# Kernel optimization log

Hardware: AMD Instinct MI355X
Metric: run time of the kernel (lower is better)

Reference implementation:

```python
import jax, jax.numpy as jnp
import numpy as np

# ---- config mirroring DetectionPostProcessV1 init + quant params ----
B, H, W, A, C = 8, 128, 128, 8, 8      # batch, feature HxW, anchors/cell, num_classes
STRIDE = 8
IMG_W, IMG_H = 1024, 1024               # image_size
INPUT_SHIFT = 4                          # kInputShift -> in_scale = 1/16
EXP_SHIFT = 4                            # from _gen_exp_table with in_scale 1/16
BOX_THR_INT = 9                          # ceil(0.55 * 2**INPUT_SHIFT)
NMS_THR = 128.0 / 256.0                  # ceil(0.5 * 2**kNmsThresholdShift) / 2**8
NMS_MARGIN = 0.0                         # nms_margin (quantized: ceil(0*16)/16)
PRE_K, POST_K = 1024, 300                # pre-NMS candidates, post_nms_top_k
CLASS_OFFSETS = jnp.zeros((C,), jnp.int32)
CLASS_SEP = 4096.0                       # coordinate offset for class-aware NMS


def setup_inputs() -> dict:
    key = jax.random.key(0)
    k1, _ = jax.random.split(key)
    # int8 repr of quantized head outputs (stored as int32 for jax indexing)
    data = jax.random.randint(k1, (B, A * (4 + C), H, W), -128, 128, dtype=jnp.int32)
    # grid anchors: 8 sizes per cell, stride-8 feature map
    sizes = np.array([16, 24, 32, 48, 64, 96, 128, 192], np.float32)
    ys = (np.arange(H, dtype=np.float32) + 0.5) * STRIDE
    xs = (np.arange(W, dtype=np.float32) + 0.5) * STRIDE
    cy, cx = np.meshgrid(ys, xs, indexing="ij")
    cx, cy = cx[..., None], cy[..., None]              # [H,W,1]
    w = np.broadcast_to(sizes, (H, W, A))
    h = np.broadcast_to(sizes, (H, W, A))
    anchors = np.stack([cx - w / 2, cy - h / 2, cx + w / 2, cy + h / 2], -1)
    anchors = jnp.asarray(anchors.reshape(-1, 4).astype(np.float32))  # [N,4] matches [H,W,A] flatten order
    # integer exp table, exactly as _gen_exp_table
    in_scale = 1.0 / (1 << INPUT_SHIFT)
    idx = np.arange(-128, 128, dtype=np.float32) * in_scale
    ev = np.exp(idx)
    exp_table = jnp.asarray(np.round(ev * (1 << EXP_SHIFT)).astype(np.int32))
    return {"data": data, "anchors": anchors, "exp_table": exp_table}


def _post_process(data, anchors, exp_table):
    N = H * W * A
    # [B, A*(4+C), H, W] -> [B, N, 4+C]
    x = data.reshape(B, A, 4 + C, H, W).transpose(0, 3, 4, 1, 2).reshape(B, N, 4 + C)
    box_d = x[..., :4]
    scores_i = x[..., 4:] + CLASS_OFFSETS                      # int scores with class offsets
    # decode: dx,dy via fixed-point shift; dw,dh via int exp table lookup
    dxy = box_d[..., :2].astype(jnp.float32) / (1 << INPUT_SHIFT)
    expv = exp_table[box_d[..., 2:4] + 128].astype(jnp.float32) / (1 << EXP_SHIFT)
    ctr = (anchors[:, :2] + anchors[:, 2:]) * 0.5              # [N,2]
    wh = anchors[:, 2:] - anchors[:, :2]
    pc = ctr + dxy * wh                                        # [B,N,2]
    pwh = wh * expv
    boxes = jnp.concatenate([pc - pwh * 0.5, pc + pwh * 0.5], -1)
    boxes = jnp.clip(boxes, 0.0, jnp.array([IMG_W, IMG_H, IMG_W, IMG_H], jnp.float32))
    # score filter
    best = scores_i.max(-1)
    label = scores_i.argmax(-1).astype(jnp.int32)
    valid = best >= BOX_THR_INT
    score = best.astype(jnp.float32) / (1 << INPUT_SHIFT)
    sc_masked = jnp.where(valid, score, -1e9)
    topv, topi = jax.lax.top_k(sc_masked, PRE_K)               # [B,PRE_K]
    bk = jnp.take_along_axis(boxes, topi[..., None], 1)        # [B,PRE_K,4]
    lk = jnp.take_along_axis(label, topi, 1)
    vk = topv > -1e8
    # class-aware NMS via coordinate offset trick
    ob = bk + lk[..., None].astype(jnp.float32) * CLASS_SEP
    area = (ob[..., 2] - ob[..., 0]) * (ob[..., 3] - ob[..., 1])
    lt = jnp.maximum(ob[:, :, None, :2], ob[:, None, :, :2])
    rb = jnp.minimum(ob[:, :, None, 2:], ob[:, None, :, 2:])
    whi = jnp.clip(rb - lt, 0.0)
    inter = whi[..., 0] * whi[..., 1]
    iou = inter / (area[:, :, None] + area[:, None, :] - inter + 1e-9)  # [B,PRE_K,PRE_K]
    idxr = jnp.arange(PRE_K)

    def body(i, sup):
        alive_i = ~jnp.take(sup, i, axis=1)                    # [B]
        iou_i = jnp.take(iou, i, axis=1)                       # [B,PRE_K]
        s_i = jnp.take(topv, i, axis=1)[:, None]
        cond = (alive_i[:, None] & (iou_i > NMS_THR)
                & (topv <= s_i - NMS_MARGIN) & (idxr > i)[None, :])
        return sup | cond

    sup = jax.lax.fori_loop(0, PRE_K, body, ~vk)
    keep = vk & ~sup
    fs = jnp.where(keep, topv, -1e9)
    outv, outi = jax.lax.top_k(fs, POST_K)
    boxes_out = jnp.take_along_axis(bk, outi[..., None], 1)
    labels = jnp.take_along_axis(lk, outi, 1)
    ok = outv > -1e8
    boxes_out = jnp.where(ok[..., None], boxes_out, 0.0)       # [B,POST_K,4]
    scores_out = jnp.where(ok, outv, 0.0)                      # [B,POST_K]
    labels_out = jnp.where(ok, labels, -1)                     # [B,POST_K]
    return boxes_out, scores_out, labels_out


def reference(data, anchors, exp_table):
    return _post_process(data, anchors, exp_table)
```

## Files before the change

kernel.cpp:

```cpp
#include <hip/hip_runtime.h>
#include <stdint.h>

#define Bb 8
#define PREK 1024
#define POSTK 300
#define NBIN 120
#define NCHUNK 512

__device__ __forceinline__ float clampb(float v){ return fminf(fmaxf(v, 0.0f), 1024.0f); }

__global__ void __launch_bounds__(256) k1_scores(const int* __restrict__ data,
                                                 unsigned short* __restrict__ sc16,
                                                 int* __restrict__ chist){
    int blk = blockIdx.x;
    int b = blk >> 7, h = blk & 127;
    int tid = threadIdx.x;
    int a = tid >> 5, wg = tid & 31;
    int w = wg << 2;
    const int* p = data + (((size_t)(b*96 + a*12 + 4)) << 14) + (h << 7) + w;
    int4 m = *(const int4*)p;
    int4 lb = make_int4(0,0,0,0);
#pragma unroll
    for (int c = 1; c < 8; ++c){
        int4 v = *(const int4*)(p + ((size_t)c << 14));
        if (v.x > m.x){ m.x = v.x; lb.x = c; }
        if (v.y > m.y){ m.y = v.y; lb.y = c; }
        if (v.z > m.z){ m.z = v.z; lb.z = c; }
        if (v.w > m.w){ m.w = v.w; lb.w = c; }
    }
    ushort4 st;
    st.x = (unsigned short)(((m.x + 128) << 8) | lb.x);
    st.y = (unsigned short)(((m.y + 128) << 8) | lb.y);
    st.z = (unsigned short)(((m.z + 128) << 8) | lb.z);
    st.w = (unsigned short)(((m.w + 128) << 8) | lb.w);
    *(ushort4*)(sc16 + (((size_t)(b*8 + a)) << 14) + (h << 7) + w) = st;

    __shared__ int hist[4][NBIN];
    for (int i = tid; i < 4*NBIN; i += 256) ((int*)hist)[i] = 0;
    __syncthreads();
    int q = wg >> 3;
    if (m.x >= 9) atomicAdd(&hist[q][m.x-9], 1);
    if (m.y >= 9) atomicAdd(&hist[q][m.y-9], 1);
    if (m.z >= 9) atomicAdd(&hist[q][m.z-9], 1);
    if (m.w >= 9) atomicAdd(&hist[q][m.w-9], 1);
    __syncthreads();
    int* cb = chist + ((size_t)(b*NCHUNK + h*4)) * NBIN;
    for (int i = tid; i < 4*NBIN; i += 256) cb[i] = ((int*)hist)[i];
}

__global__ void __launch_bounds__(256) k2_select(int* __restrict__ chist, int* __restrict__ gt,
                                                 int* __restrict__ Tb_, int* __restrict__ dmeta){
    int b = blockIdx.x, tid = threadIdx.x;
    __shared__ int hs2[2][NBIN];
    __shared__ int suf[128];
    __shared__ int Tsh;
    __shared__ int sb[512];
    if (tid == 0) Tsh = -1;
    int half = tid >> 7, bin = tid & 127;
    const int* cb = chist + (size_t)b * NCHUNK * NBIN;
    if (bin < NBIN){
        int s = 0;
        const int* p2 = cb + (size_t)half*256*NBIN + bin;
#pragma unroll 8
        for (int ch = 0; ch < 256; ++ch) s += p2[(size_t)ch * NBIN];
        hs2[half][bin] = s;
    }
    __syncthreads();
    int hbin = 0;
    if (tid < 128){
        hbin = (tid < NBIN) ? hs2[0][tid] + hs2[1][tid] : 0;
        suf[tid] = hbin;
    }
    __syncthreads();
    for (int off = 1; off < 128; off <<= 1){
        int v = 0;
        if (tid < 128 && tid + off < 128) v = suf[tid + off];
        __syncthreads();
        if (tid < 128) suf[tid] += v;
        __syncthreads();
    }
    if (tid < NBIN){
        gt[b*128 + tid] = suf[tid] - hbin;
        if (suf[tid] >= PREK) atomicMax(&Tsh, tid);
    }
    __syncthreads();
    int T = Tsh > 0 ? Tsh : 0;
    if (tid == 0) Tb_[b] = T;
    for (int k = tid; k < PREK; k += 256) dmeta[b*PREK + k] = -1;
    int i0 = tid, i1 = tid + 256;
    for (int abin = T; abin < NBIN; ++abin){
        int* basep = chist + (size_t)(b*NCHUNK) * NBIN + abin;
        int v0 = basep[(size_t)i0 * NBIN], v1 = basep[(size_t)i1 * NBIN];
        sb[i0] = v0; sb[i1] = v1;
        __syncthreads();
        for (int off = 1; off < 512; off <<= 1){
            int a0 = (i0 >= off) ? sb[i0 - off] : 0;
            int a1 = (i1 >= off) ? sb[i1 - off] : 0;
            __syncthreads();
            sb[i0] += a0; sb[i1] += a1;
            __syncthreads();
        }
        basep[(size_t)i0 * NBIN] = sb[i0] - v0;
        basep[(size_t)i1 * NBIN] = sb[i1] - v1;
        __syncthreads();
    }
}

__global__ void __launch_bounds__(256) k3_rank(const unsigned short* __restrict__ sc16,
                                               const int* __restrict__ chist,
                                               const int* __restrict__ gt, const int* __restrict__ Tb_,
                                               const int* __restrict__ data,
                                               const float* __restrict__ anchors,
                                               const int* __restrict__ etab,
                                               float4* __restrict__ dbox, int* __restrict__ dmeta){
    int blk = blockIdx.x;
    int b = blk >> 9, ci = blk & 511;
    int tid = threadIdx.x;
    int h = ci >> 2, w0 = (ci & 3) << 5;
    __shared__ unsigned short sc[256];
    __shared__ int wcnt[4][NBIN];
    if (tid < 64){
        int a = tid & 7, wq = tid >> 3;
        ushort4 v4 = *(const ushort4*)(sc16 + (((size_t)(b*8 + a)) << 14) + (h << 7) + w0 + (wq << 2));
        sc[(wq*4 + 0)*8 + a] = v4.x;
        sc[(wq*4 + 1)*8 + a] = v4.y;
        sc[(wq*4 + 2)*8 + a] = v4.z;
        sc[(wq*4 + 3)*8 + a] = v4.w;
    }
    for (int i = tid; i < 4*NBIN; i += 256) ((int*)wcnt)[i] = 0;
    int T = Tb_[b];
    __syncthreads();
    unsigned short v = sc[tid];
    int s = (int)(v >> 8) - 128;
    int bin = s - 9;
    bool qual = (bin >= T);
    int wv = tid >> 6, lane = tid & 63;
    if (qual) atomicAdd(&wcnt[wv][bin], 1);
    __syncthreads();
    int myeq = 0;
    {
        unsigned long long low = (1ull << lane) - 1ull;
        for (int vb = T; vb < NBIN; ++vb){
            unsigned long long bal = __ballot(qual && bin == vb);
            if (!bal) continue;
            if (qual && bin == vb) myeq = __popcll(bal & low);
        }
    }
    if (!qual) return;
    int cross = 0;
    for (int w2 = 0; w2 < wv; ++w2) cross += wcnt[w2][bin];
    int rank = gt[b*128 + bin] + chist[((size_t)(b*NCHUNK) + ci)*NBIN + bin] + cross + myeq;
    if (rank < PREK){
        int n = ci*256 + tid;
        int a = n & 7, wc = (n >> 3) & 127;
        const int* p = data + (((size_t)(b*96 + a*12)) << 14) + (h << 7) + wc;
        int d0 = p[0], d1 = p[1 << 14], d2 = p[2 << 14], d3 = p[3 << 14];
        float4 an = ((const float4*)anchors)[n];
        float cx = __fmul_rn(__fadd_rn(an.x, an.z), 0.5f);
        float cy = __fmul_rn(__fadd_rn(an.y, an.w), 0.5f);
        float wx = __fsub_rn(an.z, an.x), wy = __fsub_rn(an.w, an.y);
        float dx = __fmul_rn((float)d0, 0.0625f), dy = __fmul_rn((float)d1, 0.0625f);
        float ex = __fmul_rn((float)etab[d2 + 128], 0.0625f);
        float ey = __fmul_rn((float)etab[d3 + 128], 0.0625f);
        float pcx = __fadd_rn(cx, __fmul_rn(dx, wx));
        float pcy = __fadd_rn(cy, __fmul_rn(dy, wy));
        float hx = __fmul_rn(__fmul_rn(wx, ex), 0.5f);
        float hy = __fmul_rn(__fmul_rn(wy, ey), 0.5f);
        float x1 = clampb(__fsub_rn(pcx, hx)), y1 = clampb(__fsub_rn(pcy, hy));
        float x2 = clampb(__fadd_rn(pcx, hx)), y2 = clampb(__fadd_rn(pcy, hy));
        dbox[b*PREK + rank] = make_float4(x1, y1, x2, y2);
        dmeta[b*PREK + rank] = (int)v;
    }
}

__global__ void __launch_bounds__(1024) k45_nms_out(const float4* __restrict__ dbox,
                                                    const int* __restrict__ dmeta,
                                                    float* __restrict__ out){
    int b = blockIdx.x, tid = threadIdx.x, lane = tid & 63, wv = tid >> 6;
    __shared__ float X1[1024], Y1[1024], X2[1024], Y2[1024], AR[1024];
    __shared__ unsigned char KEEP[1024];
    __shared__ int wq[16][8];
    __shared__ int cbs[8], ccn[8];
    __shared__ int wcn[16];
    __shared__ int totS;

    int v = dmeta[b*PREK + tid];
    float4 bb = dbox[b*PREK + tid];
    bool valid = (v >= 0);
    int lc = valid ? (v & 255) : -1;
    float sval = valid ? __fmul_rn((float)((v >> 8) - 128), 0.0625f) : 0.0f;
    KEEP[tid] = 0;
    int win = 0;
#pragma unroll
    for (int c = 0; c < 8; ++c){
        unsigned long long bal = __ballot(lc == c);
        if (lane == 0) wq[wv][c] = __popcll(bal);
        if (lc == c) win = __popcll(bal & ((1ull << lane) - 1ull));
    }
    __syncthreads();
    if (tid < 8){
        int run = 0;
        for (int w2 = 0; w2 < 16; ++w2){ int t = wq[w2][tid]; wq[w2][tid] = run; run += t; }
        ccn[tid] = run;
    }
    __syncthreads();
    if (tid == 0){
        int run = 0;
        for (int c = 0; c < 8; ++c){ cbs[c] = run; run += ccn[c]; }
    }
    __syncthreads();
    int p = 0;
    if (valid){
        p = cbs[lc] + wq[wv][lc] + win;
        float off = (float)(lc << 12);
        float ox1 = __fadd_rn(bb.x, off), oy1 = __fadd_rn(bb.y, off);
        float ox2 = __fadd_rn(bb.z, off), oy2 = __fadd_rn(bb.w, off);
        X1[p] = ox1; Y1[p] = oy1; X2[p] = ox2; Y2[p] = oy2;
        AR[p] = __fmul_rn(__fsub_rn(ox2, ox1), __fsub_rn(oy2, oy1));
    }
    __syncthreads();

    if (wv < 8){
        int M = ccn[wv], base = cbs[wv];
        if (M > 0 && M <= 256){
            float rx1[4], ry1[4], rx2[4], ry2[4], rar[4];
#pragma unroll
            for (int g = 0; g < 4; ++g){
                int r = g*64 + lane;
                int ad = base + ((r < M) ? r : 0);
                rx1[g]=X1[ad]; ry1[g]=Y1[ad]; rx2[g]=X2[ad]; ry2[g]=Y2[ad]; rar[g]=AR[ad];
            }
            unsigned long long mk[4][4];
#pragma unroll
            for (int g = 0; g < 4; ++g)
#pragma unroll
                for (int w2 = 0; w2 < 4; ++w2) mk[g][w2] = 0ull;

#pragma unroll
            for (int jw = 0; jw < 4; ++jw){
                if (jw*64 < M){
                    int lim = M - jw*64; if (lim > 64) lim = 64;
                    for (int jl = 0; jl < lim; ++jl){
                        int j = jw*64 + jl;
                        int aj = base + j;
                        float jx1 = X1[aj], jy1 = Y1[aj], jx2 = X2[aj], jy2 = Y2[aj], jar = AR[aj];
#pragma unroll
                        for (int g = 0; g < 4; ++g){
                            if (g*64 < M){
                                int i = g*64 + lane;
                                float wx = fmaxf(__fsub_rn(fminf(rx2[g], jx2), fmaxf(rx1[g], jx1)), 0.0f);
                                float wy = fmaxf(__fsub_rn(fminf(ry2[g], jy2), fmaxf(ry1[g], jy1)), 0.0f);
                                float inter = __fmul_rn(wx, wy);
                                float den = __fadd_rn(__fsub_rn(__fadd_rn(rar[g], jar), inter), 1e-9f);
                                bool o = (__fdiv_rn(inter, den) > 0.5f) && (j > i);
                                mk[g][jw] |= o ? (1ull << jl) : 0ull;
                            }
                        }
                    }
                }
            }

            unsigned long long r0=0ull, r1=0ull, r2=0ull, r3=0ull;
#pragma unroll
            for (int iw = 0; iw < 4; ++iw){
                if (iw*64 < M){
                    int lim = M - iw*64; if (lim > 64) lim = 64;
                    for (int il = 0; il < lim; ++il){
                        unsigned long long cur = (iw==0)?r0:(iw==1)?r1:(iw==2)?r2:r3;
                        if (!((cur >> il) & 1ull)){
                            unsigned long long w0 = __shfl(mk[iw][0], il);
                            unsigned long long w1 = __shfl(mk[iw][1], il);
                            unsigned long long w2_ = __shfl(mk[iw][2], il);
                            unsigned long long w3_ = __shfl(mk[iw][3], il);
                            r0 |= w0; r1 |= w1; r2 |= w2_; r3 |= w3_;
                        }
                    }
                }
            }
#pragma unroll
            for (int g = 0; g < 4; ++g){
                int r = g*64 + lane;
                unsigned long long rg = (g==0)?r0:(g==1)?r1:(g==2)?r2:r3;
                if (r < M) KEEP[base + r] = (unsigned char)(((rg >> lane) & 1ull) ^ 1ull);
            }
        } else if (M > 256){
            for (int m = lane; m < M; m += 64) KEEP[base+m] = 0;
            for (int i = 0; i < M; ++i){
                if (KEEP[base+i]) continue;
                float xi1 = X1[base+i], yi1 = Y1[base+i];
                float xi2 = X2[base+i], yi2 = Y2[base+i], ai = AR[base+i];
                for (int j = i + 1 + lane; j < M; j += 64){
                    if (KEEP[base+j]) continue;
                    float wx = fmaxf(__fsub_rn(fminf(xi2, X2[base+j]), fmaxf(xi1, X1[base+j])), 0.0f);
                    float wy = fmaxf(__fsub_rn(fminf(yi2, Y2[base+j]), fmaxf(yi1, Y1[base+j])), 0.0f);
                    float inter = __fmul_rn(wx, wy);
                    float den = __fadd_rn(__fsub_rn(__fadd_rn(ai, AR[base+j]), inter), 1e-9f);
                    if (__fdiv_rn(inter, den) > 0.5f) KEEP[base+j] = 1;
                }
            }
            for (int m = lane; m < M; m += 64) KEEP[base+m] ^= 1;
        }
    }
    __syncthreads();

    bool kp = valid && (KEEP[p] != 0);
    unsigned long long bal = __ballot(kp);
    if (lane == 0) wcn[wv] = __popcll(bal);
    __syncthreads();
    if (tid == 0){
        int r = 0;
        for (int w2 = 0; w2 < 16; ++w2){ int t = wcn[w2]; wcn[w2] = r; r += t; }
        totS = r;
    }
    __syncthreads();
    int pos = wcn[wv] + __popcll(bal & ((1ull << lane) - 1ull));
    float* boxes  = out;
    float* scores = out + Bb*POSTK*4;
    float* labs   = out + Bb*POSTK*5;
    if (kp && pos < POSTK){
        int o = (b*POSTK + pos)*4;
        boxes[o+0] = bb.x; boxes[o+1] = bb.y; boxes[o+2] = bb.z; boxes[o+3] = bb.w;
        scores[b*POSTK + pos] = sval;
        labs[b*POSTK + pos] = (float)lc;
    }
    int tot = totS < POSTK ? totS : POSTK;
    if (tid >= tot && tid < POSTK){
        int o = (b*POSTK + tid)*4;
        boxes[o+0] = 0.f; boxes[o+1] = 0.f; boxes[o+2] = 0.f; boxes[o+3] = 0.f;
        scores[b*POSTK + tid] = 0.f;
        labs[b*POSTK + tid] = -1.0f;
    }
}

extern "C" void kernel_launch(void* const* d_in, const int* in_sizes, int n_in,
                              void* d_out, int out_size, void* d_ws, size_t ws_size,
                              hipStream_t stream) {
    const int*   data    = (const int*)d_in[0];
    const float* anchors = (const float*)d_in[1];
    const int*   etab    = (const int*)d_in[2];
    float* out = (float*)d_out;

    char* ws = (char*)d_ws;
    size_t off = 0;
    auto alloc = [&](size_t bytes)->char*{ char* p = ws + off; off += (bytes + 255) & ~(size_t)255; return p; };
    unsigned short* sc16 = (unsigned short*)alloc((size_t)Bb*8*16384*2);
    int* chist           = (int*)alloc((size_t)Bb*NCHUNK*NBIN*4);
    int* gt              = (int*)alloc((size_t)Bb*128*4);
    int* Tb_             = (int*)alloc((size_t)Bb*4);
    float4* dbox         = (float4*)alloc((size_t)Bb*PREK*16);
    int* dmeta           = (int*)alloc((size_t)Bb*PREK*4);
    (void)ws_size; (void)in_sizes; (void)n_in; (void)out_size;

    k1_scores<<<Bb*128, 256, 0, stream>>>(data, sc16, chist);
    k2_select<<<Bb, 256, 0, stream>>>(chist, gt, Tb_, dmeta);
    k3_rank<<<Bb*NCHUNK, 256, 0, stream>>>(sc16, chist, gt, Tb_, data, anchors, etab, dbox, dmeta);
    k45_nms_out<<<Bb, 1024, 0, stream>>>(dbox, dmeta, out);
}
```

Measured before the change: 153.3 us.

## Shrink NMS block to 512 threads, shuffle j-boxes, branchless suppression scan

The NMS/output kernel now runs 512 threads per block, each handling two candidates, so only the 8 per-class waves exist instead of 16 with half idle. The pairwise IoU loop reads the j-box coordinates by wave shuffle from registers instead of shared memory. Both inner loops get a fixed trip count with unroll-by-8 and a bounds guard, and the suppression scan uses a mask instead of a branch. Output compaction becomes two ballot passes with a running base, which adds extra barriers.

```diff
diff --git a/kernel.cpp b/kernel.cpp
--- a/kernel.cpp
+++ b/kernel.cpp
@@ -173,34 +173,40 @@
     }
 }
 
-__global__ void __launch_bounds__(1024) k45_nms_out(const float4* __restrict__ dbox,
-                                                    const int* __restrict__ dmeta,
-                                                    float* __restrict__ out){
+__global__ void __launch_bounds__(512, 2) k45_nms_out(const float4* __restrict__ dbox,
+                                                      const int* __restrict__ dmeta,
+                                                      float* __restrict__ out){
     int b = blockIdx.x, tid = threadIdx.x, lane = tid & 63, wv = tid >> 6;
     __shared__ float X1[1024], Y1[1024], X2[1024], Y2[1024], AR[1024];
     __shared__ unsigned char KEEP[1024];
-    __shared__ int wq[16][8];
+    __shared__ int wq[8][8], wq2[8][8];
     __shared__ int cbs[8], ccn[8];
-    __shared__ int wcn[16];
-    __shared__ int totS;
-
-    int v = dmeta[b*PREK + tid];
-    float4 bb = dbox[b*PREK + tid];
-    bool valid = (v >= 0);
-    int lc = valid ? (v & 255) : -1;
-    float sval = valid ? __fmul_rn((float)((v >> 8) - 128), 0.0625f) : 0.0f;
-    KEEP[tid] = 0;
-    int win = 0;
+    __shared__ int wcn[8];
+    __shared__ int pbase;
+
+    int v0 = dmeta[b*PREK + tid];
+    int v1 = dmeta[b*PREK + 512 + tid];
+    float4 bb0 = dbox[b*PREK + tid];
+    float4 bb1 = dbox[b*PREK + 512 + tid];
+    bool valid0 = (v0 >= 0), valid1 = (v1 >= 0);
+    int lc0 = valid0 ? (v0 & 255) : -1;
+    int lc1 = valid1 ? (v1 & 255) : -1;
+    KEEP[tid] = 0; KEEP[tid + 512] = 0;
+    if (tid == 0) pbase = 0;
+    int win0 = 0, win1 = 0;
 #pragma unroll
     for (int c = 0; c < 8; ++c){
-        unsigned long long bal = __ballot(lc == c);
-        if (lane == 0) wq[wv][c] = __popcll(bal);
-        if (lc == c) win = __popcll(bal & ((1ull << lane) - 1ull));
+        unsigned long long bal0 = __ballot(lc0 == c);
+        unsigned long long bal1 = __ballot(lc1 == c);
+        if (lane == 0){ wq[wv][c] = __popcll(bal0); wq2[wv][c] = __popcll(bal1); }
+        if (lc0 == c) win0 = __popcll(bal0 & ((1ull << lane) - 1ull));
+        if (lc1 == c) win1 = __popcll(bal1 & ((1ull << lane) - 1ull));
     }
     __syncthreads();
     if (tid < 8){
         int run = 0;
-        for (int w2 = 0; w2 < 16; ++w2){ int t = wq[w2][tid]; wq[w2][tid] = run; run += t; }
+        for (int w2 = 0; w2 < 8; ++w2){ int t = wq[w2][tid];  wq[w2][tid]  = run; run += t; }
+        for (int w2 = 0; w2 < 8; ++w2){ int t = wq2[w2][tid]; wq2[w2][tid] = run; run += t; }
         ccn[tid] = run;
     }
     __syncthreads();
@@ -209,18 +215,26 @@
         for (int c = 0; c < 8; ++c){ cbs[c] = run; run += ccn[c]; }
     }
     __syncthreads();
-    int p = 0;
-    if (valid){
-        p = cbs[lc] + wq[wv][lc] + win;
-        float off = (float)(lc << 12);
-        float ox1 = __fadd_rn(bb.x, off), oy1 = __fadd_rn(bb.y, off);
-        float ox2 = __fadd_rn(bb.z, off), oy2 = __fadd_rn(bb.w, off);
-        X1[p] = ox1; Y1[p] = oy1; X2[p] = ox2; Y2[p] = oy2;
-        AR[p] = __fmul_rn(__fsub_rn(ox2, ox1), __fsub_rn(oy2, oy1));
-    }
-    __syncthreads();
-
-    if (wv < 8){
+    int p0 = 0, p1 = 0;
+    if (valid0){
+        p0 = cbs[lc0] + wq[wv][lc0] + win0;
+        float off = (float)(lc0 << 12);
+        float ox1 = __fadd_rn(bb0.x, off), oy1 = __fadd_rn(bb0.y, off);
+        float ox2 = __fadd_rn(bb0.z, off), oy2 = __fadd_rn(bb0.w, off);
+        X1[p0] = ox1; Y1[p0] = oy1; X2[p0] = ox2; Y2[p0] = oy2;
+        AR[p0] = __fmul_rn(__fsub_rn(ox2, ox1), __fsub_rn(oy2, oy1));
+    }
+    if (valid1){
+        p1 = cbs[lc1] + wq2[wv][lc1] + win1;
+        float off = (float)(lc1 << 12);
+        float ox1 = __fadd_rn(bb1.x, off), oy1 = __fadd_rn(bb1.y, off);
+        float ox2 = __fadd_rn(bb1.z, off), oy2 = __fadd_rn(bb1.w, off);
+        X1[p1] = ox1; Y1[p1] = oy1; X2[p1] = ox2; Y2[p1] = oy2;
+        AR[p1] = __fmul_rn(__fsub_rn(ox2, ox1), __fsub_rn(oy2, oy1));
+    }
+    __syncthreads();
+
+    {
         int M = ccn[wv], base = cbs[wv];
         if (M > 0 && M <= 256){
             float rx1[4], ry1[4], rx2[4], ry2[4], rar[4];
@@ -239,21 +253,27 @@
 #pragma unroll
             for (int jw = 0; jw < 4; ++jw){
                 if (jw*64 < M){
-                    int lim = M - jw*64; if (lim > 64) lim = 64;
-                    for (int jl = 0; jl < lim; ++jl){
-                        int j = jw*64 + jl;
-                        int aj = base + j;
-                        float jx1 = X1[aj], jy1 = Y1[aj], jx2 = X2[aj], jy2 = Y2[aj], jar = AR[aj];
-#pragma unroll
-                        for (int g = 0; g < 4; ++g){
-                            if (g*64 < M){
-                                int i = g*64 + lane;
-                                float wx = fmaxf(__fsub_rn(fminf(rx2[g], jx2), fmaxf(rx1[g], jx1)), 0.0f);
-                                float wy = fmaxf(__fsub_rn(fminf(ry2[g], jy2), fmaxf(ry1[g], jy1)), 0.0f);
-                                float inter = __fmul_rn(wx, wy);
-                                float den = __fadd_rn(__fsub_rn(__fadd_rn(rar[g], jar), inter), 1e-9f);
-                                bool o = (__fdiv_rn(inter, den) > 0.5f) && (j > i);
-                                mk[g][jw] |= o ? (1ull << jl) : 0ull;
+                    int limj = M - jw*64; if (limj > 64) limj = 64;
+#pragma unroll 8
+                    for (int jl = 0; jl < 64; ++jl){
+                        if (jl < limj){
+                            int j = jw*64 + jl;
+                            float jx1 = __shfl(rx1[jw], jl);
+                            float jy1 = __shfl(ry1[jw], jl);
+                            float jx2 = __shfl(rx2[jw], jl);
+                            float jy2 = __shfl(ry2[jw], jl);
+                            float jar = __shfl(rar[jw], jl);
+#pragma unroll
+                            for (int g = 0; g < 4; ++g){
+                                if (g*64 < M){
+                                    int i = g*64 + lane;
+                                    float wx = fmaxf(__fsub_rn(fminf(rx2[g], jx2), fmaxf(rx1[g], jx1)), 0.0f);
+                                    float wy = fmaxf(__fsub_rn(fminf(ry2[g], jy2), fmaxf(ry1[g], jy1)), 0.0f);
+                                    float inter = __fmul_rn(wx, wy);
+                                    float den = __fadd_rn(__fsub_rn(__fadd_rn(rar[g], jar), inter), 1e-9f);
+                                    bool o = (__fdiv_rn(inter, den) > 0.5f) && (j > i);
+                                    mk[g][jw] |= o ? (1ull << jl) : 0ull;
+                                }
                             }
                         }
                     }
@@ -264,15 +284,17 @@
 #pragma unroll
             for (int iw = 0; iw < 4; ++iw){
                 if (iw*64 < M){
-                    int lim = M - iw*64; if (lim > 64) lim = 64;
-                    for (int il = 0; il < lim; ++il){
-                        unsigned long long cur = (iw==0)?r0:(iw==1)?r1:(iw==2)?r2:r3;
-                        if (!((cur >> il) & 1ull)){
+                    int limi = M - iw*64; if (limi > 64) limi = 64;
+#pragma unroll 8
+                    for (int il = 0; il < 64; ++il){
+                        if (il < limi){
+                            unsigned long long cur = (iw==0)?r0:(iw==1)?r1:(iw==2)?r2:r3;
                             unsigned long long w0 = __shfl(mk[iw][0], il);
                             unsigned long long w1 = __shfl(mk[iw][1], il);
                             unsigned long long w2_ = __shfl(mk[iw][2], il);
                             unsigned long long w3_ = __shfl(mk[iw][3], il);
-                            r0 |= w0; r1 |= w1; r2 |= w2_; r3 |= w3_;
+                            unsigned long long msk = ((cur >> il) & 1ull) ? 0ull : ~0ull;
+                            r0 |= w0 & msk; r1 |= w1 & msk; r2 |= w2_ & msk; r3 |= w3_ & msk;
                         }
                     }
                 }
@@ -303,27 +325,37 @@
     }
     __syncthreads();
 
-    bool kp = valid && (KEEP[p] != 0);
-    unsigned long long bal = __ballot(kp);
-    if (lane == 0) wcn[wv] = __popcll(bal);
-    __syncthreads();
-    if (tid == 0){
-        int r = 0;
-        for (int w2 = 0; w2 < 16; ++w2){ int t = wcn[w2]; wcn[w2] = r; r += t; }
-        totS = r;
-    }
-    __syncthreads();
-    int pos = wcn[wv] + __popcll(bal & ((1ull << lane) - 1ull));
     float* boxes  = out;
     float* scores = out + Bb*POSTK*4;
     float* labs   = out + Bb*POSTK*5;
-    if (kp && pos < POSTK){
-        int o = (b*POSTK + pos)*4;
-        boxes[o+0] = bb.x; boxes[o+1] = bb.y; boxes[o+2] = bb.z; boxes[o+3] = bb.w;
-        scores[b*POSTK + pos] = sval;
-        labs[b*POSTK + pos] = (float)lc;
-    }
-    int tot = totS < POSTK ? totS : POSTK;
+#pragma unroll
+    for (int pass = 0; pass < 2; ++pass){
+        bool vld   = pass ? valid1 : valid0;
+        int  pp    = pass ? p1 : p0;
+        int  lcc   = pass ? lc1 : lc0;
+        int  vv    = pass ? v1 : v0;
+        float4 bbb = pass ? bb1 : bb0;
+        bool kp = vld && (KEEP[pp] != 0);
+        unsigned long long bal = __ballot(kp);
+        if (lane == 0) wcn[wv] = __popcll(bal);
+        __syncthreads();
+        if (tid == 0){
+            int r = pbase;
+            for (int w2 = 0; w2 < 8; ++w2){ int t = wcn[w2]; wcn[w2] = r; r += t; }
+            pbase = r;
+        }
+        __syncthreads();
+        int pos = wcn[wv] + __popcll(bal & ((1ull << lane) - 1ull));
+        if (kp && pos < POSTK){
+            float sval = __fmul_rn((float)((vv >> 8) - 128), 0.0625f);
+            int o = (b*POSTK + pos)*4;
+            boxes[o+0] = bbb.x; boxes[o+1] = bbb.y; boxes[o+2] = bbb.z; boxes[o+3] = bbb.w;
+            scores[b*POSTK + pos] = sval;
+            labs[b*POSTK + pos] = (float)lcc;
+        }
+        __syncthreads();
+    }
+    int tot = pbase < POSTK ? pbase : POSTK;
     if (tid >= tot && tid < POSTK){
         int o = (b*POSTK + tid)*4;
         boxes[o+0] = 0.f; boxes[o+1] = 0.f; boxes[o+2] = 0.f; boxes[o+3] = 0.f;
@@ -354,5 +386,5 @@
     k1_scores<<<Bb*128, 256, 0, stream>>>(data, sc16, chist);
     k2_select<<<Bb, 256, 0, stream>>>(chist, gt, Tb_, dmeta);
     k3_rank<<<Bb*NCHUNK, 256, 0, stream>>>(sc16, chist, gt, Tb_, data, anchors, etab, dbox, dmeta);
-    k45_nms_out<<<Bb, 1024, 0, stream>>>(dbox, dmeta, out);
-}
+    k45_nms_out<<<Bb, 512, 0, stream>>>(dbox, dmeta, out);
+}
```

Result: no change. 156.2 us (+1.9%).

## Parallelize NMS IoU mask build across all threads and widen histogram reduction

Applied to the files above, without the earlier changes.

The NMS kernel now computes the per-class IoU suppression bitmask with one thread per box across all 1024 threads, storing rows in a shared-memory matrix. Previously one wave per class built the whole mask serially over j. The greedy sweep then reads rows from shared memory with a one-row prefetch instead of using cross-lane shuffles. Separately, the selection kernel launches 1024 threads and splits the per-bin histogram sum into 8 partial groups to shorten the serial reduction loop. The change adds 32KB of shared memory and leaves load imbalance across threads, since the inner loop length depends on each box's position within its class.

```diff
diff --git a/kernel.cpp b/kernel.cpp
--- a/kernel.cpp
+++ b/kernel.cpp
@@ -48,27 +48,35 @@
     for (int i = tid; i < 4*NBIN; i += 256) cb[i] = ((int*)hist)[i];
 }
 
-__global__ void __launch_bounds__(256) k2_select(int* __restrict__ chist, int* __restrict__ gt,
-                                                 int* __restrict__ Tb_, int* __restrict__ dmeta){
+__global__ void __launch_bounds__(1024) k2_select(int* __restrict__ chist, int* __restrict__ gt,
+                                                  int* __restrict__ Tb_, int* __restrict__ dmeta){
     int b = blockIdx.x, tid = threadIdx.x;
-    __shared__ int hs2[2][NBIN];
+    __shared__ int part[8][NBIN];
+    __shared__ int hs[NBIN];
     __shared__ int suf[128];
     __shared__ int Tsh;
     __shared__ int sb[512];
     if (tid == 0) Tsh = -1;
-    int half = tid >> 7, bin = tid & 127;
     const int* cb = chist + (size_t)b * NCHUNK * NBIN;
-    if (bin < NBIN){
+    if (tid < 8*NBIN){
+        int g = tid / NBIN, bin = tid - g*NBIN;
         int s = 0;
-        const int* p2 = cb + (size_t)half*256*NBIN + bin;
+        const int* p2 = cb + (size_t)g*64*NBIN + bin;
 #pragma unroll 8
-        for (int ch = 0; ch < 256; ++ch) s += p2[(size_t)ch * NBIN];
-        hs2[half][bin] = s;
+        for (int ch = 0; ch < 64; ++ch) s += p2[(size_t)ch * NBIN];
+        part[g][bin] = s;
+    }
+    __syncthreads();
+    if (tid < NBIN){
+        int s = 0;
+#pragma unroll
+        for (int g = 0; g < 8; ++g) s += part[g][tid];
+        hs[tid] = s;
     }
     __syncthreads();
     int hbin = 0;
     if (tid < 128){
-        hbin = (tid < NBIN) ? hs2[0][tid] + hs2[1][tid] : 0;
+        hbin = (tid < NBIN) ? hs[tid] : 0;
         suf[tid] = hbin;
     }
     __syncthreads();
@@ -86,22 +94,20 @@
     __syncthreads();
     int T = Tsh > 0 ? Tsh : 0;
     if (tid == 0) Tb_[b] = T;
-    for (int k = tid; k < PREK; k += 256) dmeta[b*PREK + k] = -1;
-    int i0 = tid, i1 = tid + 256;
+    dmeta[b*PREK + tid] = -1;
     for (int abin = T; abin < NBIN; ++abin){
         int* basep = chist + (size_t)(b*NCHUNK) * NBIN + abin;
-        int v0 = basep[(size_t)i0 * NBIN], v1 = basep[(size_t)i1 * NBIN];
-        sb[i0] = v0; sb[i1] = v1;
+        int v = 0;
+        if (tid < 512){ v = basep[(size_t)tid * NBIN]; sb[tid] = v; }
         __syncthreads();
         for (int off = 1; off < 512; off <<= 1){
-            int a0 = (i0 >= off) ? sb[i0 - off] : 0;
-            int a1 = (i1 >= off) ? sb[i1 - off] : 0;
+            int a2 = 0;
+            if (tid < 512 && tid >= off) a2 = sb[tid - off];
             __syncthreads();
-            sb[i0] += a0; sb[i1] += a1;
+            if (tid < 512) sb[tid] += a2;
             __syncthreads();
         }
-        basep[(size_t)i0 * NBIN] = sb[i0] - v0;
-        basep[(size_t)i1 * NBIN] = sb[i1] - v1;
+        if (tid < 512) basep[(size_t)tid * NBIN] = sb[tid] - v;
         __syncthreads();
     }
 }
@@ -178,6 +184,8 @@
                                                     float* __restrict__ out){
     int b = blockIdx.x, tid = threadIdx.x, lane = tid & 63, wv = tid >> 6;
     __shared__ float X1[1024], Y1[1024], X2[1024], Y2[1024], AR[1024];
+    __shared__ unsigned long long MAT[1024][4];
+    __shared__ signed char CLS[1024];
     __shared__ unsigned char KEEP[1024];
     __shared__ int wq[16][8];
     __shared__ int cbs[8], ccn[8];
@@ -190,6 +198,7 @@
     int lc = valid ? (v & 255) : -1;
     float sval = valid ? __fmul_rn((float)((v >> 8) - 128), 0.0625f) : 0.0f;
     KEEP[tid] = 0;
+    CLS[tid] = -1;
     int win = 0;
 #pragma unroll
     for (int c = 0; c < 8; ++c){
@@ -217,71 +226,70 @@
         float ox2 = __fadd_rn(bb.z, off), oy2 = __fadd_rn(bb.w, off);
         X1[p] = ox1; Y1[p] = oy1; X2[p] = ox2; Y2[p] = oy2;
         AR[p] = __fmul_rn(__fsub_rn(ox2, ox1), __fsub_rn(oy2, oy1));
+        CLS[p] = (signed char)lc;
+    }
+    __syncthreads();
+
+    {
+        int c = CLS[tid];
+        if (c >= 0){
+            int base = cbs[c], M = ccn[c];
+            if (M <= 256){
+                int i = tid - base;
+                float xi1 = X1[tid], yi1 = Y1[tid], xi2 = X2[tid], yi2 = Y2[tid], ai = AR[tid];
+                int w0 = i >> 6;
+                int NW = (M + 63) >> 6;
+#pragma unroll
+                for (int w = 0; w < 4; ++w){
+                    unsigned long long bits = 0ull;
+                    if (w >= w0 && w < NW){
+                        int jb = w << 6;
+                        int lim = M - jb; if (lim > 64) lim = 64;
+                        for (int jl = 0; jl < lim; ++jl){
+                            int j = jb + jl;
+                            if (j > i){
+                                int aj = base + j;
+                                float wx = fmaxf(__fsub_rn(fminf(xi2, X2[aj]), fmaxf(xi1, X1[aj])), 0.0f);
+                                float wy = fmaxf(__fsub_rn(fminf(yi2, Y2[aj]), fmaxf(yi1, Y1[aj])), 0.0f);
+                                float inter = __fmul_rn(wx, wy);
+                                float den = __fadd_rn(__fsub_rn(__fadd_rn(ai, AR[aj]), inter), 1e-9f);
+                                if (__fdiv_rn(inter, den) > 0.5f) bits |= (1ull << jl);
+                            }
+                        }
+                    }
+                    MAT[tid][w] = bits;
+                }
+            }
+        }
     }
     __syncthreads();
 
     if (wv < 8){
         int M = ccn[wv], base = cbs[wv];
         if (M > 0 && M <= 256){
-            float rx1[4], ry1[4], rx2[4], ry2[4], rar[4];
-#pragma unroll
-            for (int g = 0; g < 4; ++g){
-                int r = g*64 + lane;
-                int ad = base + ((r < M) ? r : 0);
-                rx1[g]=X1[ad]; ry1[g]=Y1[ad]; rx2[g]=X2[ad]; ry2[g]=Y2[ad]; rar[g]=AR[ad];
-            }
-            unsigned long long mk[4][4];
-#pragma unroll
-            for (int g = 0; g < 4; ++g)
-#pragma unroll
-                for (int w2 = 0; w2 < 4; ++w2) mk[g][w2] = 0ull;
-
-#pragma unroll
-            for (int jw = 0; jw < 4; ++jw){
-                if (jw*64 < M){
-                    int lim = M - jw*64; if (lim > 64) lim = 64;
-                    for (int jl = 0; jl < lim; ++jl){
-                        int j = jw*64 + jl;
-                        int aj = base + j;
-                        float jx1 = X1[aj], jy1 = Y1[aj], jx2 = X2[aj], jy2 = Y2[aj], jar = AR[aj];
-#pragma unroll
-                        for (int g = 0; g < 4; ++g){
-                            if (g*64 < M){
-                                int i = g*64 + lane;
-                                float wx = fmaxf(__fsub_rn(fminf(rx2[g], jx2), fmaxf(rx1[g], jx1)), 0.0f);
-                                float wy = fmaxf(__fsub_rn(fminf(ry2[g], jy2), fmaxf(ry1[g], jy1)), 0.0f);
-                                float inter = __fmul_rn(wx, wy);
-                                float den = __fadd_rn(__fsub_rn(__fadd_rn(rar[g], jar), inter), 1e-9f);
-                                bool o = (__fdiv_rn(inter, den) > 0.5f) && (j > i);
-                                mk[g][jw] |= o ? (1ull << jl) : 0ull;
-                            }
-                        }
+            int NW = (M + 63) >> 6;
+            unsigned long long rem0=0ull, rem1=0ull, rem2=0ull, rem3=0ull;
+            unsigned long long nx0 = MAT[base][0], nx1 = MAT[base][1];
+            unsigned long long nx2 = MAT[base][2], nx3 = MAT[base][3];
+            for (int iw = 0; iw < NW; ++iw){
+                int limi = M - (iw << 6); if (limi > 64) limi = 64;
+                for (int il = 0; il < limi; ++il){
+                    unsigned long long c0=nx0, c1=nx1, c2=nx2, c3=nx3;
+                    int r = base + (iw << 6) + il;
+                    int rn = (r + 1 < base + M) ? r + 1 : r;
+                    nx0 = MAT[rn][0]; nx1 = MAT[rn][1]; nx2 = MAT[rn][2]; nx3 = MAT[rn][3];
+                    unsigned long long cur = (iw==0)?rem0:(iw==1)?rem1:(iw==2)?rem2:rem3;
+                    if (!((cur >> il) & 1ull)){
+                        rem0 |= c0; rem1 |= c1; rem2 |= c2; rem3 |= c3;
                     }
                 }
             }
-
-            unsigned long long r0=0ull, r1=0ull, r2=0ull, r3=0ull;
-#pragma unroll
-            for (int iw = 0; iw < 4; ++iw){
-                if (iw*64 < M){
-                    int lim = M - iw*64; if (lim > 64) lim = 64;
-                    for (int il = 0; il < lim; ++il){
-                        unsigned long long cur = (iw==0)?r0:(iw==1)?r1:(iw==2)?r2:r3;
-                        if (!((cur >> il) & 1ull)){
-                            unsigned long long w0 = __shfl(mk[iw][0], il);
-                            unsigned long long w1 = __shfl(mk[iw][1], il);
-                            unsigned long long w2_ = __shfl(mk[iw][2], il);
-                            unsigned long long w3_ = __shfl(mk[iw][3], il);
-                            r0 |= w0; r1 |= w1; r2 |= w2_; r3 |= w3_;
-                        }
-                    }
-                }
-            }
-#pragma unroll
-            for (int g = 0; g < 4; ++g){
-                int r = g*64 + lane;
-                unsigned long long rg = (g==0)?r0:(g==1)?r1:(g==2)?r2:r3;
-                if (r < M) KEEP[base + r] = (unsigned char)(((rg >> lane) & 1ull) ^ 1ull);
+            {
+                int r = lane;
+                if (r       < M) KEEP[base+r]     = (unsigned char)(((rem0 >> lane) & 1ull) ^ 1ull);
+                if (r + 64  < M) KEEP[base+r+64]  = (unsigned char)(((rem1 >> lane) & 1ull) ^ 1ull);
+                if (r + 128 < M) KEEP[base+r+128] = (unsigned char)(((rem2 >> lane) & 1ull) ^ 1ull);
+                if (r + 192 < M) KEEP[base+r+192] = (unsigned char)(((rem3 >> lane) & 1ull) ^ 1ull);
             }
         } else if (M > 256){
             for (int m = lane; m < M; m += 64) KEEP[base+m] = 0;
@@ -352,7 +360,7 @@
     (void)ws_size; (void)in_sizes; (void)n_in; (void)out_size;
 
     k1_scores<<<Bb*128, 256, 0, stream>>>(data, sc16, chist);
-    k2_select<<<Bb, 256, 0, stream>>>(chist, gt, Tb_, dmeta);
+    k2_select<<<Bb, 1024, 0, stream>>>(chist, gt, Tb_, dmeta);
     k3_rank<<<Bb*NCHUNK, 256, 0, stream>>>(sc16, chist, gt, Tb_, data, anchors, etab, dbox, dmeta);
     k45_nms_out<<<Bb, 1024, 0, stream>>>(dbox, dmeta, out);
 }
```

New measurement: 149.6 us. 1.02x faster.
